# Optimization experiments

Hardware: AMD Instinct MI355X
Metric: run time of the kernel (lower is better)

The kernel has to match this reference:

```python
import jax, jax.numpy as jnp
import numpy as np

N_NODES = 81 * 4096   # 4096 graphs x 81 nodes (81 forced by h.view(-1,1,64*81))
N_EDGES = 4_000_000
HID = 32


def _edge_softmax(logits, mask, dst, n):
    # DGL edge_softmax restricted to masked edge subset, normalized per destination node
    NEG = jnp.float32(-1e30)
    l = jnp.where(mask, logits, NEG)
    m = jax.ops.segment_max(l, dst, num_segments=n)
    m = jnp.where(m > -1e29, m, 0.0)  # dst with no masked in-edges
    e = jnp.where(mask, jnp.exp(l - m[dst]), 0.0)
    s = jax.ops.segment_sum(e, dst, num_segments=n)
    return e / jnp.maximum(s[dst], 1e-20)


def _wsgconv(h, src, dst, w, n, W, b, bias, cs, cp, cn):
    pos = w > 0
    neg = w < 0
    a_p = _edge_softmax(w, pos, dst, n)            # softmax of w on positive subgraph
    a_n = _edge_softmax(jnp.abs(w), neg, dst, n)   # softmax of |w| on negative subgraph
    h_p = jax.ops.segment_sum(h[src] * a_p[:, None], dst, num_segments=n)
    h_n = jax.ops.segment_sum(h[src] * a_n[:, None], dst, num_segments=n)
    comb = jnp.concatenate([cs * h, cp * h_p, cn * h_n], axis=1)
    return jax.nn.relu(comb @ W.T + b + bias)


def _conv1d(x, k, stride):
    return jax.lax.conv_general_dilated(x, k, (stride,), 'VALID',
                                        dimension_numbers=('NCH', 'OIH', 'NCH'))


def reference(src, dst, w, n_nodes, W1, b1, bias1, c1s, c1p, c1n,
              W2, b2, bias2, c2s, c2p, c2n, k1, bk1, k2, bk2, Wfc, bfc, Wc, bc):
    n = n_nodes
    deg = jax.ops.segment_sum(jnp.ones_like(w), dst, num_segments=n)
    h0 = deg[:, None]                                  # in_degrees feature [N,1]
    h1 = _wsgconv(h0, src, dst, w, n, W1, b1, bias1, c1s, c1p, c1n)
    h2 = _wsgconv(h1, src, dst, w, n, W2, b2, bias2, c2s, c2p, c2n)
    h = jnp.concatenate([h1, h2], axis=1)              # JumpingKnowledge('cat') -> [N,64]
    # GSAPool(ratio=1.0) returns the input feature unchanged -> identity
    B = n // 81
    x = h.reshape(B, 1, 64 * 81)
    x = _conv1d(x, k1, 64) + bk1[None, :, None]        # [B,16,81]
    x = x[..., :80].reshape(B, 16, 40, 2).max(-1)      # MaxPool1d(2) -> [B,16,40]
    x = _conv1d(x, k2, 3) + bk2[None, :, None]         # [B,32,13]
    x = x.reshape(B, 32 * 13)
    x = jax.nn.relu(x @ Wfc.T + bfc)
    # F.dropout skipped (deterministic reference)
    logits = x @ Wc.T + bc
    return jax.nn.log_softmax(logits, axis=-1)


def setup_inputs():
    key = jax.random.key(0)
    ks = jax.random.split(key, 16)
    s = 0.1
    return {
        'src': jax.random.randint(ks[0], (N_EDGES,), 0, N_NODES),
        'dst': jax.random.randint(ks[1], (N_EDGES,), 0, N_NODES),
        'w': jax.random.normal(ks[2], (N_EDGES,), jnp.float32),
        'n_nodes': N_NODES,
        'W1': jax.random.normal(ks[3], (HID, 3), jnp.float32) * s,
        'b1': jax.random.normal(ks[4], (HID,), jnp.float32) * s,
        'bias1': jnp.zeros((HID,), jnp.float32),
        'c1s': jnp.ones((1,), jnp.float32),
        'c1p': jnp.ones((1,), jnp.float32),
        'c1n': jnp.ones((1,), jnp.float32),
        'W2': jax.random.normal(ks[5], (HID, 3 * HID), jnp.float32) * s,
        'b2': jax.random.normal(ks[6], (HID,), jnp.float32) * s,
        'bias2': jnp.zeros((HID,), jnp.float32),
        'c2s': jnp.ones((1,), jnp.float32),
        'c2p': jnp.ones((1,), jnp.float32),
        'c2n': jnp.ones((1,), jnp.float32),
        'k1': jax.random.normal(ks[7], (16, 1, 64), jnp.float32) * s,
        'bk1': jax.random.normal(ks[8], (16,), jnp.float32) * s,
        'k2': jax.random.normal(ks[9], (32, 16, 3), jnp.float32) * s,
        'bk2': jax.random.normal(ks[10], (32,), jnp.float32) * s,
        'Wfc': jax.random.normal(ks[11], (128, 32 * 13), jnp.float32) * s,
        'bfc': jax.random.normal(ks[12], (128,), jnp.float32) * s,
        'Wc': jax.random.normal(ks[13], (10, 128), jnp.float32) * s,
        'bc': jax.random.normal(ks[14], (10,), jnp.float32) * s,
    }
```

## Files before the change

### kernel.cpp

```cpp
#include <hip/hip_runtime.h>
#include <hip/hip_bf16.h>

#define NNODES 331776
#define NGRAPH 4096
#define NBUCK  2048
#define BNODES 162
#define TE     16384
#define PASSES 4
#define CAP    2560
#define CH     64
#define EB     16

typedef __attribute__((ext_vector_type(8))) short bf8;
typedef __attribute__((ext_vector_type(4))) float f4;
typedef __attribute__((ext_vector_type(4))) unsigned int u32x4;

static __device__ __forceinline__ short f2bf(float x) {
    return (short)__builtin_bit_cast(unsigned short, __float2bfloat16(x));
}
static __device__ __forceinline__ float bf2f(unsigned short u) {
    return __bfloat162float(__hip_bfloat16_raw{u});
}


__global__ __launch_bounds__(256) void k_hist(const int* __restrict__ dst,
                                              int* __restrict__ H, int E) {
    __shared__ int h[NBUCK];
    int t = threadIdx.x, b = blockIdx.x;
    for (int i = t; i < NBUCK; i += 256) h[i] = 0;
    __syncthreads();
    for (int pass = 0; pass < PASSES; pass++) {
        int lo = b * TE + pass * (EB * 256);
        int bins[EB]; bool ok[EB];
#pragma unroll
        for (int i = 0; i < EB; i++) {
            int e = lo + i * 256 + t;
            ok[i] = e < E;
            bins[i] = ok[i] ? (dst[e] / BNODES) : 0;
        }
#pragma unroll
        for (int i = 0; i < EB; i++)
            if (ok[i]) atomicAdd(&h[bins[i]], 1);
    }
    __syncthreads();
    for (int i = t; i < NBUCK; i += 256) H[b * NBUCK + i] = h[i];
}

__global__ __launch_bounds__(256) void k_colA(const int* __restrict__ H,
                                              int* __restrict__ P,
                                              int NT, int CS) {
    int idx = blockIdx.x * 256 + threadIdx.x;
    int bin = idx & (NBUCK - 1);
    int chunk = idx >> 11;
    int t0 = chunk * CS, t1 = min(NT, t0 + CS);
    int s = 0;
    for (int t = t0; t < t1; t++) s += H[t * NBUCK + bin];
    P[chunk * NBUCK + bin] = s;
}

__global__ __launch_bounds__(256) void k_colB(int* __restrict__ P,
                                              int* __restrict__ T) {
    int bin = blockIdx.x * 256 + threadIdx.x;
    int s = 0;
    for (int c = 0; c < CH; c++) {
        int v = P[c * NBUCK + bin];
        P[c * NBUCK + bin] = s;
        s += v;
    }
    T[bin] = s;
}

__global__ __launch_bounds__(256) void k_colC(int* __restrict__ H,
                                              const int* __restrict__ P,
                                              int NT, int CS) {
    int idx = blockIdx.x * 256 + threadIdx.x;
    int bin = idx & (NBUCK - 1);
    int chunk = idx >> 11;
    int t0 = chunk * CS, t1 = min(NT, t0 + CS);
    int s = P[chunk * NBUCK + bin];
    for (int t = t0; t < t1; t++) {
        int v = H[t * NBUCK + bin];
        H[t * NBUCK + bin] = s;
        s += v;
    }
}

__global__ __launch_bounds__(256) void k_binscan(const int* __restrict__ T,
                                                 int* __restrict__ Bstart) {
    __shared__ int tmp[256];
    int t = threadIdx.x;
    int base = t * 8;
    int loc[8]; int s = 0;
#pragma unroll
    for (int i = 0; i < 8; i++) { loc[i] = s; s += T[base + i]; }
    tmp[t] = s; __syncthreads();
    for (int o = 1; o < 256; o <<= 1) {
        int a = (t >= o) ? tmp[t - o] : 0;
        __syncthreads();
        tmp[t] += a;
        __syncthreads();
    }
    int excl = tmp[t] - s;
#pragma unroll
    for (int i = 0; i < 8; i++) Bstart[base + i] = excl + loc[i];
    if (t == 255) Bstart[NBUCK] = excl + s;
}

__global__ __launch_bounds__(1024) void k_place(
    const int* __restrict__ src, const int* __restrict__ dst,
    const float* __restrict__ w,
    const int* __restrict__ H, const int* __restrict__ Bstart,
    int2* __restrict__ csrB, int E) {
    __shared__ int2 pb[TE];
    __shared__ int lstart[NBUCK + 1];
    __shared__ int gshift[NBUCK];
    __shared__ int lcur[NBUCK];
    __shared__ int tsum[1024];
    int t = threadIdx.x, b = blockIdx.x;
    for (int i = t; i < NBUCK; i += 1024) lcur[i] = 0;
    __syncthreads();
    {
        int bins[16];
#pragma unroll
        for (int k = 0; k < 16; k++) {
            int e = b * TE + k * 1024 + t;
            bins[k] = (e < E) ? (dst[e] / BNODES) : -1;
        }
#pragma unroll
        for (int k = 0; k < 16; k++)
            if (bins[k] >= 0) atomicAdd(&lcur[bins[k]], 1);
    }
    __syncthreads();
    int b0 = t * 2;
    int c0 = lcur[b0], c1 = lcur[b0 + 1];
    tsum[t] = c0 + c1;
    __syncthreads();
    for (int o = 1; o < 1024; o <<= 1) {
        int a = (t >= o) ? tsum[t - o] : 0;
        __syncthreads();
        tsum[t] += a;
        __syncthreads();
    }
    int excl = tsum[t] - (c0 + c1);
    lstart[b0] = excl;
    lstart[b0 + 1] = excl + c0;
    if (t == 1023) lstart[NBUCK] = excl + c0 + c1;
    gshift[b0]     = Bstart[b0]     + H[b * NBUCK + b0]     - excl;
    gshift[b0 + 1] = Bstart[b0 + 1] + H[b * NBUCK + b0 + 1] - (excl + c0);
    lcur[b0] = excl;
    lcur[b0 + 1] = excl + c0;
    __syncthreads();
    {
        int dd[16], sx[16]; float wv[16]; bool ok[16];
#pragma unroll
        for (int k = 0; k < 16; k++) {
            int e = b * TE + k * 1024 + t;
            ok[k] = e < E;
            if (ok[k]) { dd[k] = dst[e]; sx[k] = src[e]; wv[k] = w[e]; }
        }
        int pk0[16]; float es[16]; int bin[16];
#pragma unroll
        for (int k = 0; k < 16; k++) {
            if (ok[k]) {
                float v = wv[k];
                float e2 = 0.f;
                if (v > 0.f)      e2 = __expf(v);
                else if (v < 0.f) e2 = -__expf(-v);
                es[k] = e2;
                bin[k] = dd[k] / BNODES;
                pk0[k] = sx[k] | ((dd[k] - bin[k] * BNODES) << 19);
            }
        }
        int p[16];
#pragma unroll
        for (int k = 0; k < 16; k++)
            if (ok[k]) p[k] = atomicAdd(&lcur[bin[k]], 1);
#pragma unroll
        for (int k = 0; k < 16; k++)
            if (ok[k]) {
                int2 pk; pk.x = pk0[k]; pk.y = __float_as_int(es[k]);
                pb[p[k]] = pk;
            }
    }
    __syncthreads();
    int S = lstart[NBUCK];
    for (int k = 0; k < 16; k++) {
        int i = k * 1024 + t;
        if (i < S) {
            int lo = 0, hi = NBUCK;
            while (hi - lo > 1) {
                int mid = (lo + hi) >> 1;
                if (lstart[mid] <= i) lo = mid; else hi = mid;
            }
            csrB[gshift[lo] + i] = pb[i];
        }
    }
}

__global__ __launch_bounds__(256) void k_sortbucket(
    int2* __restrict__ csrB, const int* __restrict__ Bstart,
    int* __restrict__ cnt, int* __restrict__ cntp, int* __restrict__ offs) {
    __shared__ int2 pb[CAP];
    __shared__ int lcnt[BNODES * 2];
    __shared__ int lpos[BNODES * 2];
    int t = threadIdx.x, b = blockIdx.x;
    int lo = Bstart[b];
    int S  = Bstart[b + 1] - lo;
    if (S > CAP) S = CAP;
    for (int i = t; i < BNODES * 2; i += 256) lcnt[i] = 0;
    __syncthreads();
    for (int i = t; i < S; i += 256) {
        int2 pk = csrB[lo + i];
        pb[i] = pk;
        int key = ((pk.x >> 19) << 1) | ((unsigned)pk.y >> 31);
        atomicAdd(&lcnt[key], 1);
    }
    __syncthreads();
    if (t == 0) {
        int s = 0;
        for (int i = 0; i < BNODES * 2; i++) { lpos[i] = s; s += lcnt[i]; }
    }
    __syncthreads();
    int node0 = b * BNODES;
    for (int i = t; i < BNODES; i += 256) {
        cnt[node0 + i]  = lcnt[2 * i] + lcnt[2 * i + 1];
        cntp[node0 + i] = lcnt[2 * i];
        offs[node0 + i] = lo + lpos[2 * i];
    }
    __syncthreads();
    for (int i = t; i < S; i += 256) {
        int2 pk = pb[i];
        int local = pk.x >> 19;
        int sign  = (unsigned)pk.y >> 31;
        int key = (local << 1) | sign;
        int p = atomicAdd(&lpos[key], 1);
        int d7 = (node0 + local) & 7;
        int2 outv;
        outv.x = (pk.x & 0x7FFFF) | (d7 << 19) | (sign << 22);
        outv.y = pk.y & 0x7FFFFFFF;
        csrB[lo + p] = outv;
    }
}


__global__ __launch_bounds__(256) void k_layer1(
    const int* __restrict__ cnt, const int* __restrict__ cntp,
    const int* __restrict__ offs, const int2* __restrict__ csr,
    float* __restrict__ spos, float* __restrict__ sneg,
    unsigned short* __restrict__ h1b,
    unsigned long long* __restrict__ xtab,
    const float* __restrict__ W1, const float* __restrict__ b1,
    const float* __restrict__ bias1,
    const float* __restrict__ c1s, const float* __restrict__ c1p,
    const float* __restrict__ c1n) {
    int t = threadIdx.x;
    int g = t >> 4, f = t & 15;
    int d = blockIdx.x * 16 + g;
    int beg = offs[d];
    int len = cnt[d];
    int np  = cntp[d];
    float sp = 0.f, sn = 0.f, up = 0.f, un = 0.f;
    for (int j = 0; j < len; j += 16) {
        int rem = len - j;
        if (f < rem) {
            int2 sw = csr[beg + j + f];
            float es = __int_as_float(sw.y);
            float degs = (float)cnt[sw.x & 0x7FFFF];
            float ep = (j + f < np) ? es : 0.f;
            float en = es - ep;
            sp += ep; sn += en;
            up = fmaf(degs, ep, up); un = fmaf(degs, en, un);
        }
    }
#pragma unroll
    for (int m = 8; m; m >>= 1) {
        sp += __shfl_xor(sp, m, 16);
        sn += __shfl_xor(sn, m, 16);
        up += __shfl_xor(up, m, 16);
        un += __shfl_xor(un, m, 16);
    }
    if (f == 0) { spos[d] = sp; sneg[d] = sn; }
    float hp = up / fmaxf(sp, 1e-20f);
    float hn = un / fmaxf(sn, 1e-20f);
    float x0 = c1s[0] * (float)len;
    float x1 = c1p[0] * hp;
    float x2 = c1n[0] * hn;
    if (f == 0) {
        unsigned long long u0 = (unsigned short)f2bf(x0);
        unsigned long long u1 = (unsigned short)f2bf(x1);
        unsigned long long u2 = (unsigned short)f2bf(x2);
        xtab[d] = u0 | (u1 << 16) | (u2 << 32) | (0x3F80ULL << 48);
    }
#pragma unroll
    for (int q = 0; q < 2; q++) {
        int ff = f + q * 16;
        float v = W1[ff * 3] * x0 + W1[ff * 3 + 1] * x1 + W1[ff * 3 + 2] * x2
                + b1[ff] + bias1[ff];
        v = fmaxf(v, 0.f);
        h1b[d * 32 + ff] = (unsigned short)f2bf(v);
    }
}


struct AggFront {
    int pk;
    unsigned long long r80, r81;
};

__global__ __launch_bounds__(256) void k_agg(
    const int* __restrict__ cnt, const int* __restrict__ offs,
    const int2* __restrict__ csr,
    const float* __restrict__ spos, const float* __restrict__ sneg,
    const unsigned long long* __restrict__ xtab,
    const unsigned short* __restrict__ W1Tb,
    unsigned short* __restrict__ hpb, unsigned short* __restrict__ hnb,
    int E) {
    __shared__ unsigned short Hl[4][32][40];
    __shared__ unsigned short Sl[4][16][40];
    int t = threadIdx.x;
    int wv = t >> 6, lane = t & 63;
    int col = lane & 15, quad = lane >> 4;
    int d0 = (blockIdx.x * 4 + wv) * 8;
    int beg = offs[d0];
    int totlen = 0;
#pragma unroll
    for (int i = 0; i < 8; i++) totlen += cnt[d0 + i];

    bf8 B1[2];
#pragma unroll
    for (int fh = 0; fh < 2; fh++) {
        u32x4 bw = {0u, 0u, 0u, 0u};
        if (quad == 0) {
            int n = fh * 16 + col;
            unsigned w0 = W1Tb[0 * 32 + n], w1 = W1Tb[1 * 32 + n];
            unsigned w2 = W1Tb[2 * 32 + n], w3 = W1Tb[3 * 32 + n];
            bw.x = w0 | (w1 << 16);
            bw.y = w2 | (w3 << 16);
        }
        B1[fh] = __builtin_bit_cast(bf8, bw);
    }

    f4 acc2[2] = {{0.f, 0.f, 0.f, 0.f}, {0.f, 0.f, 0.f, 0.f}};
    unsigned short (*myH)[40] = Hl[wv];
    unsigned short (*myS)[40] = Sl[wv];
    int nw = (totlen + 31) >> 5;

    auto LDREC = [&](int w) -> long long {
        int eidx = w * 32 + (lane & 31);
        int gidx = beg + ((eidx < totlen) ? eidx : 0);
        gidx = gidx < E ? gidx : E - 1;
        return *(const long long*)(csr + gidx);
    };
    auto DERIVE = [&](long long rec, int w, AggFront& f) {
        int x = (int)rec;
        float ef = __int_as_float((int)(rec >> 32));
        int eidx = w * 32 + (lane & 31);
        int slot = (eidx < totlen) ? (((x >> 19) & 7) * 2 + ((x >> 22) & 1)) : 255;
        unsigned es16 = (unsigned)(unsigned short)f2bf(ef);
        f.pk = (int)(es16 | ((unsigned)slot << 16));
        int xm0 = __builtin_amdgcn_ds_bpermute(col * 4, x);
        int xm1 = __builtin_amdgcn_ds_bpermute((16 + col) * 4, x);
        f.r80 = 0; f.r81 = 0;
        if (quad == 0) {
            f.r80 = xtab[(unsigned)xm0 & 0x7FFFF];
            f.r81 = xtab[(unsigned)xm1 & 0x7FFFF];
        }
    };

    if (nw > 0) {
        AggFront fc, fn;
        long long rec0 = LDREC(0);
        DERIVE(rec0, 0, fc);
        long long recN = (nw > 1) ? LDREC(1) : rec0;

        for (int w = 0; w < nw; w++) {
            long long recNN = (w + 2 < nw) ? LDREC(w + 2) : recN;
            if (w + 1 < nw) DERIVE(recN, w + 1, fn);
            recN = recNN;

            int slot = ((unsigned)fc.pk >> 16);
            unsigned short es16 = (unsigned short)(fc.pk & 0xFFFF);
            {
                u32x4 z = {0u, 0u, 0u, 0u};
                *(u32x4*)&myS[lane >> 2][(lane & 3) * 8] = z;
            }
            if (lane < 32 && slot < 16)
                myS[slot][lane & 31] = es16;

#pragma unroll
            for (int eh = 0; eh < 2; eh++) {
                unsigned long long r8 = eh ? fc.r81 : fc.r80;
                u32x4 av = {(unsigned)r8, (unsigned)(r8 >> 32), 0u, 0u};
                bf8 A1 = __builtin_bit_cast(bf8, av);
#pragma unroll
                for (int fh = 0; fh < 2; fh++) {
                    f4 h = {0.f, 0.f, 0.f, 0.f};
                    h = __builtin_amdgcn_mfma_f32_16x16x32_bf16(A1, B1[fh], h, 0, 0, 0);
                    float l0 = fmaxf(h[0], 0.f), h0 = fmaxf(h[1], 0.f);
                    float l1 = fmaxf(h[2], 0.f), h1 = fmaxf(h[3], 0.f);
                    unsigned u0, u1;
                    asm("v_cvt_pk_bf16_f32 %0, %1, %2" : "=v"(u0) : "v"(l0), "v"(h0));
                    asm("v_cvt_pk_bf16_f32 %0, %1, %2" : "=v"(u1) : "v"(l1), "v"(h1));
                    *(unsigned long long*)&myH[fh * 16 + col][eh * 16 + quad * 4] =
                        (unsigned long long)u0 | ((unsigned long long)u1 << 32);
                }
            }

            bf8 A2 = *(const bf8*)&myS[col][quad * 8];

#pragma unroll
            for (int fh = 0; fh < 2; fh++) {
                bf8 B2 = *(const bf8*)&myH[fh * 16 + col][quad * 8];
                acc2[fh] = __builtin_amdgcn_mfma_f32_16x16x32_bf16(A2, B2, acc2[fh], 0, 0, 0);
            }
            fc = fn;
        }
    }

#pragma unroll
    for (int i = 0; i < 4; i++) {
        int slot = quad * 4 + i;
        int node = d0 + (slot >> 1);
        float s = (slot & 1) ? sneg[node] : spos[node];
        float r = 1.0f / fmaxf(s, 1e-20f);
        unsigned short* bp = (slot & 1) ? hnb : hpb;
#pragma unroll
        for (int fh = 0; fh < 2; fh++) {
            float v = acc2[fh][i] * r;
            bp[(size_t)node * 32 + fh * 16 + col] = (unsigned short)f2bf(v);
        }
    }
}


__global__ __launch_bounds__(256) void k_prep(
    const float* __restrict__ W2, const float* __restrict__ c2s,
    const float* __restrict__ c2p, const float* __restrict__ c2n,
    const float* __restrict__ k1,
    const float* __restrict__ W1, const float* __restrict__ b1,
    const float* __restrict__ bias1,
    unsigned short* __restrict__ W2sT, unsigned short* __restrict__ k1T,
    unsigned short* __restrict__ W1Tb) {
    int i = blockIdx.x * 256 + threadIdx.x;
    if (i < 96 * 32) {
        int k = i >> 5, n = i & 31;
        float sc = (k < 32) ? c2s[0] : ((k < 64) ? c2p[0] : c2n[0]);
        W2sT[i] = (unsigned short)f2bf(W2[n * 96 + k] * sc);
    } else if (i < 96 * 32 + 64 * 16) {
        int j = i - 3072;
        int k = j >> 4, o = j & 15;
        k1T[j] = (unsigned short)f2bf(k1[o * 64 + k]);
    } else if (i < 96 * 32 + 64 * 16 + 4 * 32) {
        int j = i - (3072 + 1024);
        int k = j >> 5, n = j & 31;
        float v = (k < 3) ? W1[n * 3 + k] : (b1[n] + bias1[n]);
        W1Tb[j] = (unsigned short)f2bf(v);
    }
}


__global__ __launch_bounds__(256) void k_mlp_mfma(
    const unsigned short* __restrict__ h1b,
    const unsigned short* __restrict__ hpb, const unsigned short* __restrict__ hnb,
    const unsigned short* __restrict__ W2sT, const unsigned short* __restrict__ k1T,
    const float* __restrict__ b2, const float* __restrict__ bias2,
    const float* __restrict__ bk1,
    float* __restrict__ y1) {
    __shared__ unsigned short h2s[4][16 * 32];
    int t = threadIdx.x;
    int wv = t >> 6;
    int lane = t & 63;
    int col = lane & 15;
    int quad = lane >> 4;

    float bv0 = b2[col] + bias2[col];
    float bv1 = b2[col + 16] + bias2[col + 16];
    float bky = bk1[col];

    bf8 BW[2][3];
#pragma unroll
    for (int nt = 0; nt < 2; nt++)
#pragma unroll
        for (int kt = 0; kt < 3; kt++) {
            bf8 b;
#pragma unroll
            for (int j = 0; j < 8; j++)
                b[j] = (short)W2sT[(kt * 32 + quad * 8 + j) * 32 + nt * 16 + col];
            BW[nt][kt] = b;
        }
    bf8 BK[2];
#pragma unroll
    for (int kt = 0; kt < 2; kt++) {
        bf8 b;
#pragma unroll
        for (int j = 0; j < 8; j++)
            b[j] = (short)k1T[(kt * 32 + quad * 8 + j) * 16 + col];
        BK[kt] = b;
    }
    unsigned short* myT = h2s[wv];

#pragma unroll 1
    for (int g = 0; g < 4; g++) {
        int nbase = blockIdx.x * 256 + wv * 64 + g * 16;
        int node = nbase + col;
        bf8 a0 = *(const bf8*)(h1b + (size_t)node * 32 + quad * 8);
        bf8 a1 = *(const bf8*)(hpb + (size_t)node * 32 + quad * 8);
        bf8 a2 = *(const bf8*)(hnb + (size_t)node * 32 + quad * 8);

        f4 acc0 = {bv0, bv0, bv0, bv0};
        f4 acc1 = {bv1, bv1, bv1, bv1};
        acc0 = __builtin_amdgcn_mfma_f32_16x16x32_bf16(a0, BW[0][0], acc0, 0, 0, 0);
        acc0 = __builtin_amdgcn_mfma_f32_16x16x32_bf16(a1, BW[0][1], acc0, 0, 0, 0);
        acc0 = __builtin_amdgcn_mfma_f32_16x16x32_bf16(a2, BW[0][2], acc0, 0, 0, 0);
        acc1 = __builtin_amdgcn_mfma_f32_16x16x32_bf16(a0, BW[1][0], acc1, 0, 0, 0);
        acc1 = __builtin_amdgcn_mfma_f32_16x16x32_bf16(a1, BW[1][1], acc1, 0, 0, 0);
        acc1 = __builtin_amdgcn_mfma_f32_16x16x32_bf16(a2, BW[1][2], acc1, 0, 0, 0);

#pragma unroll
        for (int i = 0; i < 4; i++) {
            int r = quad * 4 + i;
            myT[r * 32 + col]      = (unsigned short)f2bf(fmaxf(acc0[i], 0.f));
            myT[r * 32 + col + 16] = (unsigned short)f2bf(fmaxf(acc1[i], 0.f));
        }
        bf8 ah2 = *(const bf8*)(myT + col * 32 + quad * 8);

        f4 accy = {bky, bky, bky, bky};
        accy = __builtin_amdgcn_mfma_f32_16x16x32_bf16(a0,  BK[0], accy, 0, 0, 0);
        accy = __builtin_amdgcn_mfma_f32_16x16x32_bf16(ah2, BK[1], accy, 0, 0, 0);
#pragma unroll
        for (int i = 0; i < 4; i++)
            y1[(size_t)(nbase + quad * 4 + i) * 16 + col] = accy[i];
    }
}


__global__ void k_transpose(const float* __restrict__ Wfc, float* __restrict__ W4) {
    int i = blockIdx.x * 256 + threadIdx.x;
    if (i < 128 * 416) {
        int u = i / 416, c = i - u * 416;
        W4[(c >> 2) * 512 + u * 4 + (c & 3)] = Wfc[i];
    }
}


__global__ __launch_bounds__(256) void k_head(
    const float* __restrict__ y1, const float* __restrict__ k2,
    const float* __restrict__ bk2, const float* __restrict__ W4,
    const float* __restrict__ bfc, const float* __restrict__ Wc,
    const float* __restrict__ bc, float* __restrict__ out) {
    __shared__ float yl[1296];
    __shared__ float zl[16][41];
    __shared__ float xr[416];
    __shared__ float k2s[1536];
    __shared__ float fl2[256];
    __shared__ float fl[128];
    __shared__ float ll[10];
    int t = threadIdx.x;
    int b = blockIdx.x;
    const float4* yb4 = (const float4*)(y1 + (size_t)b * 1296);
    for (int i = t; i < 324; i += 256) ((float4*)yl)[i] = yb4[i];
    for (int i = t; i < 1536; i += 256) k2s[i] = k2[i];
    __syncthreads();
    for (int i = t; i < 640; i += 256) {
        int ic = i & 15, p = i >> 4;
        zl[ic][p] = fmaxf(yl[(2 * p) * 16 + ic], yl[(2 * p + 1) * 16 + ic]);
    }
    __syncthreads();
    for (int i = t; i < 416; i += 256) {
        int oc = i / 13, tt = i - oc * 13;
        float acc = bk2[oc];
        for (int ic = 0; ic < 16; ic++) {
            const float* kk = &k2s[(oc * 16 + ic) * 3];
            acc += zl[ic][3 * tt]     * kk[0]
                 + zl[ic][3 * tt + 1] * kk[1]
                 + zl[ic][3 * tt + 2] * kk[2];
        }
        xr[i] = acc;
    }
    __syncthreads();
    {
        int u = t & 127, q = t >> 7;
        float acc = 0.f;
        const float4* xr4 = (const float4*)xr;
        for (int i4 = q * 52; i4 < q * 52 + 52; i4++) {
            float4 wv = *(const float4*)(W4 + i4 * 512 + u * 4);
            float4 xv = xr4[i4];
            acc = fmaf(xv.x, wv.x, acc);
            acc = fmaf(xv.y, wv.y, acc);
            acc = fmaf(xv.z, wv.z, acc);
            acc = fmaf(xv.w, wv.w, acc);
        }
        fl2[t] = acc;
    }
    __syncthreads();
    if (t < 128)
        fl[t] = fmaxf(fl2[t] + fl2[t + 128] + bfc[t], 0.f);
    __syncthreads();
    if (t < 160) {
        int c = t >> 4, l = t & 15;
        float acc = 0.f;
        for (int i = l * 8; i < l * 8 + 8; i++)
            acc += fl[i] * Wc[c * 128 + i];
        for (int m = 8; m; m >>= 1) acc += __shfl_down(acc, m, 16);
        if (l == 0) ll[c] = acc + bc[c];
    }
    __syncthreads();
    if (t < 10) {
        float m = -1e30f;
        for (int c = 0; c < 10; c++) m = fmaxf(m, ll[c]);
        float s = 0.f;
        for (int c = 0; c < 10; c++) s += __expf(ll[c] - m);
        out[b * 10 + t] = ll[t] - m - __logf(s);
    }
}


extern "C" void kernel_launch(void* const* d_in, const int* in_sizes, int n_in,
                              void* d_out, int out_size, void* d_ws, size_t ws_size,
                              hipStream_t stream) {
    const int*   src   = (const int*)d_in[0];
    const int*   dst   = (const int*)d_in[1];
    const float* w     = (const float*)d_in[2];
    const float* W1    = (const float*)d_in[4];
    const float* b1    = (const float*)d_in[5];
    const float* bias1 = (const float*)d_in[6];
    const float* c1s   = (const float*)d_in[7];
    const float* c1p   = (const float*)d_in[8];
    const float* c1n   = (const float*)d_in[9];
    const float* W2    = (const float*)d_in[10];
    const float* b2    = (const float*)d_in[11];
    const float* bias2 = (const float*)d_in[12];
    const float* c2s   = (const float*)d_in[13];
    const float* c2p   = (const float*)d_in[14];
    const float* c2n   = (const float*)d_in[15];
    const float* k1    = (const float*)d_in[16];
    const float* bk1   = (const float*)d_in[17];
    const float* k2    = (const float*)d_in[18];
    const float* bk2   = (const float*)d_in[19];
    const float* Wfc   = (const float*)d_in[20];
    const float* bfc   = (const float*)d_in[21];
    const float* Wc    = (const float*)d_in[22];
    const float* bc    = (const float*)d_in[23];
    const int E = in_sizes[0];
    const int NT = (E + TE - 1) / TE;
    const int CS = (NT + CH - 1) / CH;

    size_t off = 0;
    auto carve = [&](size_t bytes) -> char* {
        char* p = (char*)d_ws + off;
        off = (off + bytes + 255) & ~(size_t)255;
        return p;
    };
    int*   cnt    = (int*)  carve((size_t)NNODES * 4);
    int*   cntp   = (int*)  carve((size_t)NNODES * 4);
    int*   offs   = (int*)  carve((size_t)NNODES * 4);
    int2*  csrB   = (int2*) carve((size_t)E * 8);
    int*   H      = (int*)  carve((size_t)NT * NBUCK * 4);
    int*   P      = (int*)  carve((size_t)CH * NBUCK * 4);
    int*   T      = (int*)  carve((size_t)NBUCK * 4);
    int*   Bstart = (int*)  carve((size_t)(NBUCK + 1) * 4);
    float* spos   = (float*)carve((size_t)NNODES * 4);
    float* sneg   = (float*)carve((size_t)NNODES * 4);
    unsigned short* h1b = (unsigned short*)carve((size_t)NNODES * 32 * 2);
    unsigned short* hpb = (unsigned short*)carve((size_t)NNODES * 32 * 2);
    unsigned short* hnb = (unsigned short*)carve((size_t)NNODES * 32 * 2);
    float* y1     = (float*)carve((size_t)NNODES * 16 * 4);
    float* WfcT   = (float*)carve((size_t)128 * 416 * 4);
    unsigned short* W2sT = (unsigned short*)carve((size_t)96 * 32 * 2);
    unsigned short* k1T  = (unsigned short*)carve((size_t)64 * 16 * 2);
    unsigned short* W1Tb = (unsigned short*)carve((size_t)4 * 32 * 2);
    unsigned long long* xtab = (unsigned long long*)y1;
    (void)ws_size;

    k_hist      <<<NT, 256, 0, stream>>>(dst, H, E);
    k_colA      <<<CH * NBUCK / 256, 256, 0, stream>>>(H, P, NT, CS);
    k_colB      <<<NBUCK / 256, 256, 0, stream>>>(P, T);
    k_colC      <<<CH * NBUCK / 256, 256, 0, stream>>>(H, P, NT, CS);
    k_binscan   <<<1, 256, 0, stream>>>(T, Bstart);
    k_place     <<<NT, 1024, 0, stream>>>(src, dst, w, H, Bstart, csrB, E);
    k_sortbucket<<<NBUCK, 256, 0, stream>>>(csrB, Bstart, cnt, cntp, offs);
    k_layer1    <<<NNODES / 16, 256, 0, stream>>>(cnt, cntp, offs, csrB,
                                                  spos, sneg, h1b, xtab,
                                                  W1, b1, bias1, c1s, c1p, c1n);
    k_prep      <<<17, 256, 0, stream>>>(W2, c2s, c2p, c2n, k1,
                                         W1, b1, bias1, W2sT, k1T, W1Tb);
    k_transpose <<<(128 * 416 + 255) / 256, 256, 0, stream>>>(Wfc, WfcT);
    k_agg       <<<NNODES / 32, 256, 0, stream>>>(cnt, offs, csrB,
                                                  spos, sneg, xtab, W1Tb,
                                                  hpb, hnb, E);
    k_mlp_mfma  <<<NNODES / 256, 256, 0, stream>>>(h1b, hpb, hnb, W2sT, k1T,
                                                   b2, bias2, bk1, y1);
    k_head      <<<NGRAPH, 256, 0, stream>>>(y1, k2, bk2, WfcT, bfc, Wc, bc,
                                             (float*)d_out);
}
```

Before: 356.7 us.

## Batch eight graphs per head block to reuse FC weight loads

The classifier head kernel now processes eight graphs per block instead of one. Each fc weight float4 is loaded once and applied to all eight graphs' conv outputs held in shared memory, which cuts global weight traffic by about eightfold. The grid shrinks to 512 blocks, and the conv2 stage runs serially per graph inside the block. This lowers parallelism and adds extra barriers and register pressure.

```diff
diff --git a/kernel.cpp b/kernel.cpp
--- a/kernel.cpp
+++ b/kernel.cpp
@@ -10,6 +10,7 @@
 #define CAP    2560
 #define CH     64
 #define EB     16
+#define GH     8
 
 typedef __attribute__((ext_vector_type(8))) short bf8;
 typedef __attribute__((ext_vector_type(4))) float f4;
@@ -550,67 +551,86 @@
     const float* __restrict__ bc, float* __restrict__ out) {
     __shared__ float yl[1296];
     __shared__ float zl[16][41];
-    __shared__ float xr[416];
     __shared__ float k2s[1536];
-    __shared__ float fl2[256];
-    __shared__ float fl[128];
-    __shared__ float ll[10];
+    __shared__ float xr_all[GH][416];
+    __shared__ float fl2s[2][128 * GH];
+    __shared__ float fl_all[GH][128];
+    __shared__ float ll[GH][10];
     int t = threadIdx.x;
-    int b = blockIdx.x;
-    const float4* yb4 = (const float4*)(y1 + (size_t)b * 1296);
-    for (int i = t; i < 324; i += 256) ((float4*)yl)[i] = yb4[i];
+    int b0 = blockIdx.x * GH;
     for (int i = t; i < 1536; i += 256) k2s[i] = k2[i];
-    __syncthreads();
-    for (int i = t; i < 640; i += 256) {
-        int ic = i & 15, p = i >> 4;
-        zl[ic][p] = fmaxf(yl[(2 * p) * 16 + ic], yl[(2 * p + 1) * 16 + ic]);
-    }
-    __syncthreads();
-    for (int i = t; i < 416; i += 256) {
-        int oc = i / 13, tt = i - oc * 13;
-        float acc = bk2[oc];
-        for (int ic = 0; ic < 16; ic++) {
-            const float* kk = &k2s[(oc * 16 + ic) * 3];
-            acc += zl[ic][3 * tt]     * kk[0]
-                 + zl[ic][3 * tt + 1] * kk[1]
-                 + zl[ic][3 * tt + 2] * kk[2];
-        }
-        xr[i] = acc;
+    for (int g = 0; g < GH; g++) {
+        const float4* yb4 = (const float4*)(y1 + (size_t)(b0 + g) * 1296);
+        __syncthreads();
+        for (int i = t; i < 324; i += 256) ((float4*)yl)[i] = yb4[i];
+        __syncthreads();
+        for (int i = t; i < 640; i += 256) {
+            int ic = i & 15, p = i >> 4;
+            zl[ic][p] = fmaxf(yl[(2 * p) * 16 + ic], yl[(2 * p + 1) * 16 + ic]);
+        }
+        __syncthreads();
+        for (int i = t; i < 416; i += 256) {
+            int oc = i / 13, tt = i - oc * 13;
+            float acc = bk2[oc];
+            for (int ic = 0; ic < 16; ic++) {
+                const float* kk = &k2s[(oc * 16 + ic) * 3];
+                acc += zl[ic][3 * tt]     * kk[0]
+                     + zl[ic][3 * tt + 1] * kk[1]
+                     + zl[ic][3 * tt + 2] * kk[2];
+            }
+            xr_all[g][i] = acc;
+        }
     }
     __syncthreads();
     {
         int u = t & 127, q = t >> 7;
-        float acc = 0.f;
-        const float4* xr4 = (const float4*)xr;
-        for (int i4 = q * 52; i4 < q * 52 + 52; i4++) {
-            float4 wv = *(const float4*)(W4 + i4 * 512 + u * 4);
-            float4 xv = xr4[i4];
-            acc = fmaf(xv.x, wv.x, acc);
-            acc = fmaf(xv.y, wv.y, acc);
-            acc = fmaf(xv.z, wv.z, acc);
-            acc = fmaf(xv.w, wv.w, acc);
-        }
-        fl2[t] = acc;
-    }
-    __syncthreads();
-    if (t < 128)
-        fl[t] = fmaxf(fl2[t] + fl2[t + 128] + bfc[t], 0.f);
+        const float* Wb = W4 + u * 4;
+        float acc[GH];
+#pragma unroll
+        for (int g = 0; g < GH; g++) acc[g] = 0.f;
+        int base = q * 52;
+#pragma unroll 2
+        for (int i4 = base; i4 < base + 52; i4++) {
+            float4 wv = *(const float4*)(Wb + (size_t)i4 * 512);
+#pragma unroll
+            for (int g = 0; g < GH; g++) {
+                float4 xv = *(const float4*)&xr_all[g][i4 * 4];
+                acc[g] = fmaf(xv.x, wv.x,
+                         fmaf(xv.y, wv.y,
+                         fmaf(xv.z, wv.z, fmaf(xv.w, wv.w, acc[g]))));
+            }
+        }
+#pragma unroll
+        for (int g = 0; g < GH; g++) fl2s[q][u * GH + g] = acc[g];
+    }
+    __syncthreads();
+    if (t < 128) {
+        float bv = bfc[t];
+#pragma unroll
+        for (int g = 0; g < GH; g++)
+            fl_all[g][t] = fmaxf(fl2s[0][t * GH + g] + fl2s[1][t * GH + g] + bv, 0.f);
+    }
     __syncthreads();
     if (t < 160) {
         int c = t >> 4, l = t & 15;
-        float acc = 0.f;
-        for (int i = l * 8; i < l * 8 + 8; i++)
-            acc += fl[i] * Wc[c * 128 + i];
-        for (int m = 8; m; m >>= 1) acc += __shfl_down(acc, m, 16);
-        if (l == 0) ll[c] = acc + bc[c];
-    }
-    __syncthreads();
-    if (t < 10) {
+        for (int g = 0; g < GH; g++) {
+            float acc = 0.f;
+            const float* fl = fl_all[g];
+            for (int i = l * 8; i < l * 8 + 8; i++)
+                acc += fl[i] * Wc[c * 128 + i];
+            for (int m = 8; m; m >>= 1) acc += __shfl_down(acc, m, 16);
+            if (l == 0) ll[g][c] = acc + bc[c];
+        }
+    }
+    __syncthreads();
+    if (t < GH * 10) {
+        int g = t / 10, c = t - g * 10;
+        const float* lg = ll[g];
         float m = -1e30f;
-        for (int c = 0; c < 10; c++) m = fmaxf(m, ll[c]);
+        for (int k = 0; k < 10; k++) m = fmaxf(m, lg[k]);
         float s = 0.f;
-        for (int c = 0; c < 10; c++) s += __expf(ll[c] - m);
-        out[b * 10 + t] = ll[t] - m - __logf(s);
+        for (int k = 0; k < 10; k++) s += __expf(lg[k] - m);
+        out[(b0 + g) * 10 + c] = lg[c] - m - __logf(s);
     }
 }
 
@@ -690,6 +710,6 @@
                                                   hpb, hnb, E);
     k_mlp_mfma  <<<NNODES / 256, 256, 0, stream>>>(h1b, hpb, hnb, W2sT, k1T,
                                                    b2, bias2, bk1, y1);
-    k_head      <<<NGRAPH, 256, 0, stream>>>(y1, k2, bk2, WfcT, bfc, Wc, bc,
-                                             (float*)d_out);
-}
+    k_head      <<<NGRAPH / GH, 256, 0, stream>>>(y1, k2, bk2, WfcT, bfc, Wc, bc,
+                                                  (float*)d_out);
+}
```

After: 349.9 us. No clear change (-1.9%).
